# Kernel tuning notes

Hardware: AMD Instinct MI355X
Metric: run time of the kernel (lower is better)

## Reference

```python
import jax, jax.numpy as jnp
import numpy as np

B, N, DIN, DOUT = 32, 1024, 256, 256


def setup_inputs() -> dict:
    key = jax.random.key(0)
    ks = jax.random.split(key, 7)
    s = 1.0 / np.sqrt(DIN)
    return {
        "x": jax.random.normal(ks[0], (B, N, DIN), dtype=jnp.float32),
        "Wq": jax.random.uniform(ks[1], (DOUT, DIN), minval=-s, maxval=s, dtype=jnp.float32),
        "bq": jax.random.uniform(ks[2], (DOUT,), minval=-s, maxval=s, dtype=jnp.float32),
        "Wk": jax.random.uniform(ks[3], (DOUT, DIN), minval=-s, maxval=s, dtype=jnp.float32),
        "bk": jax.random.uniform(ks[4], (DOUT,), minval=-s, maxval=s, dtype=jnp.float32),
        "Wv": jax.random.uniform(ks[5], (DOUT, DIN), minval=-s, maxval=s, dtype=jnp.float32),
        "bv": jax.random.uniform(ks[6], (DOUT,), minval=-s, maxval=s, dtype=jnp.float32),
    }


def reference(x, Wq, bq, Wk, bk, Wv, bv):
    # q, k, v: (B, N, Dout)
    q = jnp.einsum("bnd,od->bno", x, Wq) + bq
    k = jnp.einsum("bnd,od->bno", x, Wk) + bk
    v = jnp.einsum("bnd,od->bno", x, Wv) + bv
    # logits: (B, N, N) = q @ k^T per batch
    logits = jnp.einsum("bnd,bmd->bnm", q, k)
    # NOTE: softmax over the BATCH dim (axis=0), as in the original module
    attn = jax.nn.softmax(logits, axis=0)
    out = jnp.einsum("bnm,bmd->bnd", attn, v)  # (B, N, Dout)
    return out
```

## Files before the change

kernel.cpp:

```cpp
#include <hip/hip_runtime.h>

typedef __bf16 bf16x8 __attribute__((ext_vector_type(8)));
typedef __bf16 bf16x4 __attribute__((ext_vector_type(4)));
typedef float  f32x4  __attribute__((ext_vector_type(4)));

#define BK  64
#define LSD 144

__device__ __forceinline__ void g2l16(const void* g, void* l) {
    __builtin_amdgcn_global_load_lds((const __attribute__((address_space(1))) void*)g,
                                     (__attribute__((address_space(3))) void*)l, 16, 0, 0);
}


__global__ __launch_bounds__(256)
void gemm_proj(const float* __restrict__ x,
               const float* __restrict__ Wq, const float* __restrict__ Wk,
               const float* __restrict__ Wv,
               const float* __restrict__ bq, const float* __restrict__ bk,
               const float* __restrict__ bv,
               __bf16* __restrict__ qkv)
{
    __shared__ __align__(16) __bf16 smem[128 * LSD];
    __bf16* As = smem;
    __bf16* Bs = smem + 128 * BK;

    const int tid  = threadIdx.x;
    const int w    = tid >> 6;
    const int lane = tid & 63;
    const int quad = lane >> 4;
    const int l16  = lane & 15;
    const int wm   = w & 1;
    const int wn   = w >> 1;

    const int m0 = blockIdx.x * 128;
    const int n0 = blockIdx.y * 128;
    const int z  = blockIdx.z;

    const float* W    = z == 0 ? Wq : (z == 1 ? Wk : Wv);
    const float* bias = z == 0 ? bq : (z == 1 ? bk : bv);

    const int srow = (w << 3) + (lane >> 3);
    const int scol = ((lane & 7) ^ (lane >> 3)) << 3;
    char* ldsA = (char*)As + w * 1024 + lane * 16;
    char* ldsB = (char*)Bs + w * 1024 + lane * 16;

    const float* Ag = x + (size_t)(m0 + srow) * 256 + scol;
    const float* Bg = W + (size_t)(n0 + srow) * 256 + scol;

    f32x4 acc[4][4] = {};

    for (int k0 = 0; k0 < 256; k0 += BK) {
        __syncthreads();
        #pragma unroll
        for (int c = 0; c < 4; c++) {
            const float* s = Ag + (size_t)(c * 32) * 256 + k0;
            const float4 f0 = *(const float4*)s, f1 = *(const float4*)(s + 4);
            bf16x8 o;
            o[0] = (__bf16)f0.x; o[1] = (__bf16)f0.y; o[2] = (__bf16)f0.z; o[3] = (__bf16)f0.w;
            o[4] = (__bf16)f1.x; o[5] = (__bf16)f1.y; o[6] = (__bf16)f1.z; o[7] = (__bf16)f1.w;
            *(bf16x8*)(ldsA + c * 4096) = o;
        }
        #pragma unroll
        for (int c = 0; c < 4; c++) {
            const float* s = Bg + (size_t)(c * 32) * 256 + k0;
            const float4 f0 = *(const float4*)s, f1 = *(const float4*)(s + 4);
            bf16x8 o;
            o[0] = (__bf16)f0.x; o[1] = (__bf16)f0.y; o[2] = (__bf16)f0.z; o[3] = (__bf16)f0.w;
            o[4] = (__bf16)f1.x; o[5] = (__bf16)f1.y; o[6] = (__bf16)f1.z; o[7] = (__bf16)f1.w;
            *(bf16x8*)(ldsB + c * 4096) = o;
        }
        __syncthreads();

        #pragma unroll
        for (int kk = 0; kk < BK; kk += 32) {
            const int ub = kk >> 3;
            bf16x8 a[4], b[4];
            #pragma unroll
            for (int mt = 0; mt < 4; mt++) {
                const int row = wm * 64 + mt * 16 + l16;
                const int cp  = ((quad + ub) ^ (row & 7)) << 3;
                a[mt] = *(const bf16x8*)&As[row * BK + cp];
            }
            #pragma unroll
            for (int nt = 0; nt < 4; nt++) {
                const int row = wn * 64 + nt * 16 + l16;
                const int cp  = ((quad + ub) ^ (row & 7)) << 3;
                b[nt] = *(const bf16x8*)&Bs[row * BK + cp];
            }
            #pragma unroll
            for (int mt = 0; mt < 4; mt++)
                #pragma unroll
                for (int nt = 0; nt < 4; nt++)
                    acc[mt][nt] = __builtin_amdgcn_mfma_f32_16x16x32_bf16(
                        a[mt], b[nt], acc[mt][nt], 0, 0, 0);
        }
    }

    __syncthreads();
    if (z < 2) {
        #pragma unroll
        for (int mt = 0; mt < 4; mt++) {
            const int rl = wm * 64 + mt * 16 + quad * 4;
            #pragma unroll
            for (int nt = 0; nt < 4; nt++) {
                const int cl = wn * 64 + nt * 16 + l16;
                const float bn = bias[n0 + cl];
                #pragma unroll
                for (int r = 0; r < 4; r++)
                    smem[(rl + r) * LSD + cl] = (__bf16)(acc[mt][nt][r] + bn);
            }
        }
        __syncthreads();
        __bf16* C = qkv + (size_t)z * 8388608;
        #pragma unroll
        for (int i = 0; i < 8; i++) {
            const int c   = tid + i * 256;
            const int row = c >> 4, c8 = (c & 15) << 3;
            *(bf16x8*)&C[(size_t)(m0 + row) * 256 + n0 + c8] =
                *(const bf16x8*)&smem[row * LSD + c8];
        }
    } else {
        #pragma unroll
        for (int mt = 0; mt < 4; mt++) {
            const int ml = wm * 64 + mt * 16 + quad * 4;
            #pragma unroll
            for (int nt = 0; nt < 4; nt++) {
                const int dl = wn * 64 + nt * 16 + l16;
                const float bn = bias[n0 + dl];
                bf16x4 pk;
                #pragma unroll
                for (int r = 0; r < 4; r++) pk[r] = (__bf16)(acc[mt][nt][r] + bn);
                *(bf16x4*)&smem[dl * LSD + ml] = pk;
            }
        }
        __syncthreads();
        __bf16* C = qkv + 2 * 8388608;
        const int bidx = m0 >> 10, mbase = m0 & 1023;
        #pragma unroll
        for (int i = 0; i < 8; i++) {
            const int c  = tid + i * 256;
            const int dl = c >> 4, m8 = (c & 15) << 3;
            *(bf16x8*)&C[(size_t)bidx * 262144 + (size_t)(n0 + dl) * 1024 + mbase + m8] =
                *(const bf16x8*)&smem[dl * LSD + m8];
        }
    }
}

__global__ __launch_bounds__(256)
void gemm_logits(const __bf16* __restrict__ Q, const __bf16* __restrict__ Km,
                 __bf16* __restrict__ E)
{
    __shared__ __align__(16) __bf16 smem[128 * LSD];
    __bf16* As = smem;
    __bf16* Bs = smem + 128 * BK;

    const int tid  = threadIdx.x;
    const int w    = tid >> 6;
    const int lane = tid & 63;
    const int quad = lane >> 4;
    const int l16  = lane & 15;
    const int wm   = w & 1;
    const int wn   = w >> 1;

    const int id = blockIdx.x;
    const int x  = id & 7, s = id >> 3;
    const int z  = x + ((s >> 6) << 3);
    const int t  = s & 63;
    const int m0 = (t & 7) * 128;
    const int n0 = (t >> 3) * 128;

    const __bf16* Ab = Q  + (size_t)z * 262144;
    const __bf16* Bb = Km + (size_t)z * 262144;

    const int srow = (w << 3) + (lane >> 3);
    const int scol = ((lane & 7) ^ (lane >> 3)) << 3;
    char* ldsA = (char*)As + (size_t)w * 1024;
    char* ldsB = (char*)Bs + (size_t)w * 1024;

    const __bf16* Ag = Ab + (size_t)(m0 + srow) * 256 + scol;
    const __bf16* Bg = Bb + (size_t)(n0 + srow) * 256 + scol;

    f32x4 acc[4][4] = {};

    for (int k0 = 0; k0 < 256; k0 += BK) {
        __syncthreads();
        #pragma unroll
        for (int c = 0; c < 4; c++)
            g2l16(Ag + (size_t)(c * 32) * 256 + k0, ldsA + c * 4096);
        #pragma unroll
        for (int c = 0; c < 4; c++)
            g2l16(Bg + (size_t)(c * 32) * 256 + k0, ldsB + c * 4096);
        __syncthreads();

        #pragma unroll
        for (int kk = 0; kk < BK; kk += 32) {
            const int ub = kk >> 3;
            bf16x8 a[4], b[4];
            #pragma unroll
            for (int mt = 0; mt < 4; mt++) {
                const int row = wm * 64 + mt * 16 + l16;
                const int cp  = ((quad + ub) ^ (row & 7)) << 3;
                a[mt] = *(const bf16x8*)&As[row * BK + cp];
            }
            #pragma unroll
            for (int nt = 0; nt < 4; nt++) {
                const int row = wn * 64 + nt * 16 + l16;
                const int cp  = ((quad + ub) ^ (row & 7)) << 3;
                b[nt] = *(const bf16x8*)&Bs[row * BK + cp];
            }
            #pragma unroll
            for (int mt = 0; mt < 4; mt++)
                #pragma unroll
                for (int nt = 0; nt < 4; nt++)
                    acc[mt][nt] = __builtin_amdgcn_mfma_f32_16x16x32_bf16(
                        a[mt], b[nt], acc[mt][nt], 0, 0, 0);
        }
    }

    __syncthreads();
    #pragma unroll
    for (int mt = 0; mt < 4; mt++) {
        const int rl = wm * 64 + mt * 16 + quad * 4;
        #pragma unroll
        for (int nt = 0; nt < 4; nt++) {
            const int cl = wn * 64 + nt * 16 + l16;
            #pragma unroll
            for (int r = 0; r < 4; r++)
                smem[(rl + r) * LSD + cl] = (__bf16)__expf(acc[mt][nt][r]);
        }
    }
    __syncthreads();
    __bf16* C = E + (size_t)z * 1048576;
    #pragma unroll
    for (int i = 0; i < 8; i++) {
        const int c   = tid + i * 256;
        const int row = c >> 4, c8 = (c & 15) << 3;
        *(bf16x8*)&C[(size_t)(m0 + row) * 1024 + n0 + c8] =
            *(const bf16x8*)&smem[row * LSD + c8];
    }
}

__global__ __launch_bounds__(256)
void sum_rcp(const __bf16* __restrict__ E, __bf16* __restrict__ rcpS)
{
    const size_t p = (size_t)blockIdx.x * 256 + threadIdx.x;
    const bf16x8* E8 = (const bf16x8*)E;
    float s[8] = {0.f, 0.f, 0.f, 0.f, 0.f, 0.f, 0.f, 0.f};
    #pragma unroll
    for (int b = 0; b < 32; b++) {
        const bf16x8 e = E8[(size_t)b * 131072 + p];
        #pragma unroll
        for (int j = 0; j < 8; j++) s[j] += (float)e[j];
    }
    bf16x8 o;
    #pragma unroll
    for (int j = 0; j < 8; j++) o[j] = (__bf16)__builtin_amdgcn_rcpf(s[j]);
    ((bf16x8*)rcpS)[p] = o;
}

__global__ __launch_bounds__(256)
void gemm_pv(const __bf16* __restrict__ E, const __bf16* __restrict__ rcpS,
             const __bf16* __restrict__ vT, float* __restrict__ out)
{
    __shared__ __align__(16) __bf16 As[128 * BK];
    __shared__ __align__(16) __bf16 Bs[128 * BK];

    const int tid  = threadIdx.x;
    const int w    = tid >> 6;
    const int lane = tid & 63;
    const int quad = lane >> 4;
    const int l16  = lane & 15;
    const int wm   = w & 1;
    const int wn   = w >> 1;

    const int id = blockIdx.x;
    const int x  = id & 7, s = id >> 3;
    const int z  = x + ((s >> 4) << 3);
    const int t  = s & 15;
    const int m0 = (t & 7) * 128;
    const int n0 = (t >> 3) * 128;

    const __bf16* Eb = E  + (size_t)z * 1048576;
    const __bf16* Vb = vT + (size_t)z * 262144;
    float*        Ob = out + (size_t)z * 262144;

    const int srow = (w << 3) + (lane >> 3);
    const int scol = ((lane & 7) ^ (lane >> 3)) << 3;
    char* ldsAw = (char*)As + w * 1024 + lane * 16;
    char* ldsB  = (char*)Bs + (size_t)w * 1024;

    const __bf16* Ag = Eb   + (size_t)(m0 + srow) * 1024 + scol;
    const __bf16* Rg = rcpS + (size_t)(m0 + srow) * 1024 + scol;
    const __bf16* Bg = Vb   + (size_t)(n0 + srow) * 1024 + scol;

    f32x4 acc[4][4] = {};

    for (int k0 = 0; k0 < 1024; k0 += BK) {
        __syncthreads();
        #pragma unroll
        for (int c = 0; c < 4; c++) {
            const bf16x8 e  = *(const bf16x8*)(Ag + (size_t)(c * 32) * 1024 + k0);
            const bf16x8 rs = *(const bf16x8*)(Rg + (size_t)(c * 32) * 1024 + k0);
            bf16x8 o;
            #pragma unroll
            for (int j = 0; j < 8; j++) o[j] = (__bf16)((float)e[j] * (float)rs[j]);
            *(bf16x8*)(ldsAw + c * 4096) = o;
        }
        #pragma unroll
        for (int c = 0; c < 4; c++)
            g2l16(Bg + (size_t)(c * 32) * 1024 + k0, ldsB + c * 4096);
        __syncthreads();

        #pragma unroll
        for (int kk = 0; kk < BK; kk += 32) {
            const int ub = kk >> 3;
            bf16x8 a[4], b[4];
            #pragma unroll
            for (int mt = 0; mt < 4; mt++) {
                const int row = wm * 64 + mt * 16 + l16;
                const int cp  = ((quad + ub) ^ (row & 7)) << 3;
                a[mt] = *(const bf16x8*)&As[row * BK + cp];
            }
            #pragma unroll
            for (int nt = 0; nt < 4; nt++) {
                const int row = wn * 64 + nt * 16 + l16;
                const int cp  = ((quad + ub) ^ (row & 7)) << 3;
                b[nt] = *(const bf16x8*)&Bs[row * BK + cp];
            }
            #pragma unroll
            for (int mt = 0; mt < 4; mt++)
                #pragma unroll
                for (int nt = 0; nt < 4; nt++)
                    acc[mt][nt] = __builtin_amdgcn_mfma_f32_16x16x32_bf16(
                        a[mt], b[nt], acc[mt][nt], 0, 0, 0);
        }
    }

    #pragma unroll
    for (int mt = 0; mt < 4; mt++) {
        const int mb = m0 + wm * 64 + mt * 16 + quad * 4;
        #pragma unroll
        for (int nt = 0; nt < 4; nt++) {
            const int n = n0 + wn * 64 + nt * 16 + l16;
            #pragma unroll
            for (int r = 0; r < 4; r++)
                Ob[(size_t)(mb + r) * 256 + n] = acc[mt][nt][r];
        }
    }
}

extern "C" void kernel_launch(void* const* d_in, const int* in_sizes, int n_in,
                              void* d_out, int out_size, void* d_ws, size_t ws_size,
                              hipStream_t stream)
{
    const float* x  = (const float*)d_in[0];
    const float* Wq = (const float*)d_in[1];
    const float* bq = (const float*)d_in[2];
    const float* Wk = (const float*)d_in[3];
    const float* bk = (const float*)d_in[4];
    const float* Wv = (const float*)d_in[5];
    const float* bv = (const float*)d_in[6];
    float* out = (float*)d_out;

    char* ws = (char*)d_ws;
    __bf16* rcpS = (__bf16*)ws;
    __bf16* qkv  = (__bf16*)(ws + (16u << 20));
    __bf16* E    = (__bf16*)(ws + (64u << 20));

    gemm_proj<<<dim3(256, 2, 3), 256, 0, stream>>>(x, Wq, Wk, Wv, bq, bk, bv, qkv);

    gemm_logits<<<2048, 256, 0, stream>>>(qkv, qkv + 8388608, E);

    sum_rcp<<<512, 256, 0, stream>>>(E, rcpS);

    gemm_pv<<<512, 256, 0, stream>>>(E, rcpS, qkv + 2 * 8388608, out);
}
```

Measured before the change: 202.9 us.

## Pre-convert inputs to bf16, use direct LDS loads in projection, halve PV tile

```diff
diff --git a/kernel.cpp b/kernel.cpp
--- a/kernel.cpp
+++ b/kernel.cpp
@@ -4,8 +4,7 @@
 typedef __bf16 bf16x4 __attribute__((ext_vector_type(4)));
 typedef float  f32x4  __attribute__((ext_vector_type(4)));
 
-#define BK  64
-#define LSD 144
+#define BK 64
 
 __device__ __forceinline__ void g2l16(const void* g, void* l) {
     __builtin_amdgcn_global_load_lds((const __attribute__((address_space(1))) void*)g,
@@ -14,14 +13,10 @@
 
 
 __global__ __launch_bounds__(256)
-void gemm_proj(const float* __restrict__ x,
-               const float* __restrict__ Wq, const float* __restrict__ Wk,
-               const float* __restrict__ Wv,
-               const float* __restrict__ bq, const float* __restrict__ bk,
-               const float* __restrict__ bv,
-               __bf16* __restrict__ qkv)
-{
-    __shared__ __align__(16) __bf16 smem[128 * LSD];
+void gemm_proj(const __bf16* __restrict__ A, const __bf16* __restrict__ Wb,
+               __bf16* __restrict__ qkv, const float* __restrict__ bpack)
+{
+    __shared__ __align__(16) __bf16 smem[128 * 128];
     __bf16* As = smem;
     __bf16* Bs = smem + 128 * BK;
 
@@ -37,39 +32,27 @@
     const int n0 = blockIdx.y * 128;
     const int z  = blockIdx.z;
 
-    const float* W    = z == 0 ? Wq : (z == 1 ? Wk : Wv);
-    const float* bias = z == 0 ? bq : (z == 1 ? bk : bv);
+    const __bf16* Bb   = Wb + (size_t)z * 131072;
+    const float*  bias = bpack + z * 256;
 
     const int srow = (w << 3) + (lane >> 3);
     const int scol = ((lane & 7) ^ (lane >> 3)) << 3;
-    char* ldsA = (char*)As + w * 1024 + lane * 16;
-    char* ldsB = (char*)Bs + w * 1024 + lane * 16;
-
-    const float* Ag = x + (size_t)(m0 + srow) * 256 + scol;
-    const float* Bg = W + (size_t)(n0 + srow) * 256 + scol;
+    char* ldsA = (char*)As + (size_t)w * 1024;
+    char* ldsB = (char*)Bs + (size_t)w * 1024;
+
+    const __bf16* Ag = A  + (size_t)(m0 + srow) * 256 + scol;
+    const __bf16* Bg = Bb + (size_t)(n0 + srow) * 256 + scol;
 
     f32x4 acc[4][4] = {};
 
     for (int k0 = 0; k0 < 256; k0 += BK) {
         __syncthreads();
         #pragma unroll
-        for (int c = 0; c < 4; c++) {
-            const float* s = Ag + (size_t)(c * 32) * 256 + k0;
-            const float4 f0 = *(const float4*)s, f1 = *(const float4*)(s + 4);
-            bf16x8 o;
-            o[0] = (__bf16)f0.x; o[1] = (__bf16)f0.y; o[2] = (__bf16)f0.z; o[3] = (__bf16)f0.w;
-            o[4] = (__bf16)f1.x; o[5] = (__bf16)f1.y; o[6] = (__bf16)f1.z; o[7] = (__bf16)f1.w;
-            *(bf16x8*)(ldsA + c * 4096) = o;
-        }
-        #pragma unroll
-        for (int c = 0; c < 4; c++) {
-            const float* s = Bg + (size_t)(c * 32) * 256 + k0;
-            const float4 f0 = *(const float4*)s, f1 = *(const float4*)(s + 4);
-            bf16x8 o;
-            o[0] = (__bf16)f0.x; o[1] = (__bf16)f0.y; o[2] = (__bf16)f0.z; o[3] = (__bf16)f0.w;
-            o[4] = (__bf16)f1.x; o[5] = (__bf16)f1.y; o[6] = (__bf16)f1.z; o[7] = (__bf16)f1.w;
-            *(bf16x8*)(ldsB + c * 4096) = o;
-        }
+        for (int c = 0; c < 4; c++)
+            g2l16(Ag + (size_t)(c * 32) * 256 + k0, ldsA + c * 4096);
+        #pragma unroll
+        for (int c = 0; c < 4; c++)
+            g2l16(Bg + (size_t)(c * 32) * 256 + k0, ldsB + c * 4096);
         __syncthreads();
 
         #pragma unroll
@@ -107,8 +90,11 @@
                 const int cl = wn * 64 + nt * 16 + l16;
                 const float bn = bias[n0 + cl];
                 #pragma unroll
-                for (int r = 0; r < 4; r++)
-                    smem[(rl + r) * LSD + cl] = (__bf16)(acc[mt][nt][r] + bn);
+                for (int r = 0; r < 4; r++) {
+                    const int row = rl + r;
+                    smem[row * 128 + ((((cl >> 3) ^ (row & 7)) << 3) | (cl & 7))] =
+                        (__bf16)(acc[mt][nt][r] + bn);
+                }
             }
         }
         __syncthreads();
@@ -116,9 +102,9 @@
         #pragma unroll
         for (int i = 0; i < 8; i++) {
             const int c   = tid + i * 256;
-            const int row = c >> 4, c8 = (c & 15) << 3;
-            *(bf16x8*)&C[(size_t)(m0 + row) * 256 + n0 + c8] =
-                *(const bf16x8*)&smem[row * LSD + c8];
+            const int row = c >> 4, u = c & 15;
+            *(bf16x8*)&C[(size_t)(m0 + row) * 256 + n0 + u * 8] =
+                *(const bf16x8*)&smem[row * 128 + ((u ^ (row & 7)) << 3)];
         }
     } else {
         #pragma unroll
@@ -131,7 +117,7 @@
                 bf16x4 pk;
                 #pragma unroll
                 for (int r = 0; r < 4; r++) pk[r] = (__bf16)(acc[mt][nt][r] + bn);
-                *(bf16x4*)&smem[dl * LSD + ml] = pk;
+                *(bf16x4*)&smem[dl * 128 + ((((ml >> 3) ^ (dl & 7)) << 3) | (ml & 7))] = pk;
             }
         }
         __syncthreads();
@@ -140,9 +126,9 @@
         #pragma unroll
         for (int i = 0; i < 8; i++) {
             const int c  = tid + i * 256;
-            const int dl = c >> 4, m8 = (c & 15) << 3;
-            *(bf16x8*)&C[(size_t)bidx * 262144 + (size_t)(n0 + dl) * 1024 + mbase + m8] =
-                *(const bf16x8*)&smem[dl * LSD + m8];
+            const int dl = c >> 4, u = c & 15;
+            *(bf16x8*)&C[(size_t)bidx * 262144 + (size_t)(n0 + dl) * 1024 + mbase + u * 8] =
+                *(const bf16x8*)&smem[dl * 128 + ((u ^ (dl & 7)) << 3)];
         }
     }
 }
@@ -151,7 +137,7 @@
 void gemm_logits(const __bf16* __restrict__ Q, const __bf16* __restrict__ Km,
                  __bf16* __restrict__ E)
 {
-    __shared__ __align__(16) __bf16 smem[128 * LSD];
+    __shared__ __align__(16) __bf16 smem[128 * 128];
     __bf16* As = smem;
     __bf16* Bs = smem + 128 * BK;
 
@@ -226,8 +212,11 @@
         for (int nt = 0; nt < 4; nt++) {
             const int cl = wn * 64 + nt * 16 + l16;
             #pragma unroll
-            for (int r = 0; r < 4; r++)
-                smem[(rl + r) * LSD + cl] = (__bf16)__expf(acc[mt][nt][r]);
+            for (int r = 0; r < 4; r++) {
+                const int row = rl + r;
+                smem[row * 128 + ((((cl >> 3) ^ (row & 7)) << 3) | (cl & 7))] =
+                    (__bf16)__expf(acc[mt][nt][r]);
+            }
         }
     }
     __syncthreads();
@@ -235,9 +224,9 @@
     #pragma unroll
     for (int i = 0; i < 8; i++) {
         const int c   = tid + i * 256;
-        const int row = c >> 4, c8 = (c & 15) << 3;
-        *(bf16x8*)&C[(size_t)(m0 + row) * 1024 + n0 + c8] =
-            *(const bf16x8*)&smem[row * LSD + c8];
+        const int row = c >> 4, u = c & 15;
+        *(bf16x8*)&C[(size_t)(m0 + row) * 1024 + n0 + u * 8] =
+            *(const bf16x8*)&smem[row * 128 + ((u ^ (row & 7)) << 3)];
     }
 }
 
@@ -264,7 +253,7 @@
              const __bf16* __restrict__ vT, float* __restrict__ out)
 {
     __shared__ __align__(16) __bf16 As[128 * BK];
-    __shared__ __align__(16) __bf16 Bs[128 * BK];
+    __shared__ __align__(16) __bf16 Bs[64 * BK];
 
     const int tid  = threadIdx.x;
     const int w    = tid >> 6;
@@ -276,10 +265,10 @@
 
     const int id = blockIdx.x;
     const int x  = id & 7, s = id >> 3;
-    const int z  = x + ((s >> 4) << 3);
-    const int t  = s & 15;
+    const int z  = x + ((s >> 5) << 3);
+    const int t  = s & 31;
     const int m0 = (t & 7) * 128;
-    const int n0 = (t >> 3) * 128;
+    const int n0 = (t >> 3) * 64;
 
     const __bf16* Eb = E  + (size_t)z * 1048576;
     const __bf16* Vb = vT + (size_t)z * 262144;
@@ -294,7 +283,7 @@
     const __bf16* Rg = rcpS + (size_t)(m0 + srow) * 1024 + scol;
     const __bf16* Bg = Vb   + (size_t)(n0 + srow) * 1024 + scol;
 
-    f32x4 acc[4][4] = {};
+    f32x4 acc[4][2] = {};
 
     for (int k0 = 0; k0 < 1024; k0 += BK) {
         __syncthreads();
@@ -308,14 +297,14 @@
             *(bf16x8*)(ldsAw + c * 4096) = o;
         }
         #pragma unroll
-        for (int c = 0; c < 4; c++)
+        for (int c = 0; c < 2; c++)
             g2l16(Bg + (size_t)(c * 32) * 1024 + k0, ldsB + c * 4096);
         __syncthreads();
 
         #pragma unroll
         for (int kk = 0; kk < BK; kk += 32) {
             const int ub = kk >> 3;
-            bf16x8 a[4], b[4];
+            bf16x8 a[4], b[2];
             #pragma unroll
             for (int mt = 0; mt < 4; mt++) {
                 const int row = wm * 64 + mt * 16 + l16;
@@ -323,15 +312,15 @@
                 a[mt] = *(const bf16x8*)&As[row * BK + cp];
             }
             #pragma unroll
-            for (int nt = 0; nt < 4; nt++) {
-                const int row = wn * 64 + nt * 16 + l16;
+            for (int nt = 0; nt < 2; nt++) {
+                const int row = wn * 32 + nt * 16 + l16;
                 const int cp  = ((quad + ub) ^ (row & 7)) << 3;
                 b[nt] = *(const bf16x8*)&Bs[row * BK + cp];
             }
             #pragma unroll
             for (int mt = 0; mt < 4; mt++)
                 #pragma unroll
-                for (int nt = 0; nt < 4; nt++)
+                for (int nt = 0; nt < 2; nt++)
                     acc[mt][nt] = __builtin_amdgcn_mfma_f32_16x16x32_bf16(
                         a[mt], b[nt], acc[mt][nt], 0, 0, 0);
         }
@@ -341,12 +330,42 @@
     for (int mt = 0; mt < 4; mt++) {
         const int mb = m0 + wm * 64 + mt * 16 + quad * 4;
         #pragma unroll
-        for (int nt = 0; nt < 4; nt++) {
-            const int n = n0 + wn * 64 + nt * 16 + l16;
+        for (int nt = 0; nt < 2; nt++) {
+            const int n = n0 + wn * 32 + nt * 16 + l16;
             #pragma unroll
             for (int r = 0; r < 4; r++)
                 Ob[(size_t)(mb + r) * 256 + n] = acc[mt][nt][r];
         }
+    }
+}
+
+__global__ __launch_bounds__(256)
+void cvt_all(const float* __restrict__ x,
+             const float* __restrict__ Wq, const float* __restrict__ Wk,
+             const float* __restrict__ Wv,
+             const float* __restrict__ bq, const float* __restrict__ bk,
+             const float* __restrict__ bv,
+             __bf16* __restrict__ xb, __bf16* __restrict__ Wqb,
+             float* __restrict__ bpack)
+{
+    const int i = blockIdx.x * 256 + threadIdx.x;
+    if (i < 1073152) {
+        const float* s; __bf16* d; int off;
+        if (i < 1048576)      { s = x;  d = xb;            off = i; }
+        else if (i < 1056768) { s = Wq; d = Wqb;           off = i - 1048576; }
+        else if (i < 1064960) { s = Wk; d = Wqb + 131072;  off = i - 1056768; }
+        else                  { s = Wv; d = Wqb + 262144;  off = i - 1064960; }
+        const float4* s4 = (const float4*)s;
+        const float4 f0 = s4[off * 2], f1 = s4[off * 2 + 1];
+        bf16x8 o;
+        o[0] = (__bf16)f0.x; o[1] = (__bf16)f0.y; o[2] = (__bf16)f0.z; o[3] = (__bf16)f0.w;
+        o[4] = (__bf16)f1.x; o[5] = (__bf16)f1.y; o[6] = (__bf16)f1.z; o[7] = (__bf16)f1.w;
+        ((bf16x8*)d)[off] = o;
+    } else if (i < 1073344) {
+        const int j = i - 1073152;
+        const int sel = j >> 6, jj = j & 63;
+        const float* s = sel == 0 ? bq : (sel == 1 ? bk : bv);
+        ((float4*)bpack)[j] = ((const float4*)s)[jj];
     }
 }
 
@@ -365,14 +384,19 @@
 
     char* ws = (char*)d_ws;
     __bf16* rcpS = (__bf16*)ws;
-    __bf16* qkv  = (__bf16*)(ws + (16u << 20));
-    __bf16* E    = (__bf16*)(ws + (64u << 20));
-
-    gemm_proj<<<dim3(256, 2, 3), 256, 0, stream>>>(x, Wq, Wk, Wv, bq, bk, bv, qkv);
+    __bf16* xb   = (__bf16*)(ws + (2u  << 20));
+    __bf16* qkv  = (__bf16*)(ws + (18u << 20));
+    __bf16* E    = (__bf16*)(ws + (66u << 20));
+    __bf16* Wqb  = (__bf16*)(ws + (130u << 20));
+    float*  bpack = (float*)(ws + (130u << 20) + (1u << 20));
+
+    cvt_all<<<4194, 256, 0, stream>>>(x, Wq, Wk, Wv, bq, bk, bv, xb, Wqb, bpack);
+
+    gemm_proj<<<dim3(256, 2, 3), 256, 0, stream>>>(xb, Wqb, qkv, bpack);
 
     gemm_logits<<<2048, 256, 0, stream>>>(qkv, qkv + 8388608, E);
 
     sum_rcp<<<512, 256, 0, stream>>>(E, rcpS);
 
-    gemm_pv<<<512, 256, 0, stream>>>(E, rcpS, qkv + 2 * 8388608, out);
-}
+    gemm_pv<<<1024, 256, 0, stream>>>(E, rcpS, qkv + 2 * 8388608, out);
+}
```

After: 197.4 us. -2.7%, faster.
